# Kernel optimization log

Measured on AMD Instinct MI355X. Metric: run time of the kernel, lower is better.

Reference implementation:

```python
import jax, jax.numpy as jnp
import numpy as np

D_MODEL = 256
N_HEAD = 8
D_FF = 1024
B = 8
N_PER = 4096
NQ = B * N_PER
L = 16
NEG_INF = -1e9
EPS = 1e-5


def layer_norm(x, g, b):
    mu = jnp.mean(x, axis=-1, keepdims=True)
    var = jnp.mean(jnp.square(x - mu), axis=-1, keepdims=True)
    return (x - mu) * jax.lax.rsqrt(var + EPS) * g + b


def setup_inputs() -> dict:
    key = jax.random.key(0)
    ks = jax.random.split(key, 20)
    s = 1.0 / np.sqrt(D_MODEL)
    sf = 1.0 / np.sqrt(D_FF)
    inp = {
        "src": jax.random.normal(ks[0], (NQ, D_MODEL), jnp.float32),
        "pos": jax.random.normal(ks[1], (NQ, D_MODEL), jnp.float32),
        # per-batch-relative neighbor indices in [-1, N_PER); -1 == invalid/padded
        "index_pair": jax.random.randint(ks[2], (NQ, L), 0, N_PER + 1, jnp.int32) - 1,
        "query_batch_cnt": jnp.full((B,), N_PER, jnp.int32),
        "key_batch_cnt": jnp.full((B,), N_PER, jnp.int32),
        "index_pair_batch": (jnp.arange(NQ, dtype=jnp.int32) // N_PER).astype(jnp.int32),
        "Wq": jax.random.normal(ks[3], (D_MODEL, D_MODEL), jnp.float32) * s,
        "bq": jnp.zeros((D_MODEL,), jnp.float32),
        "Wk": jax.random.normal(ks[4], (D_MODEL, D_MODEL), jnp.float32) * s,
        "bk": jnp.zeros((D_MODEL,), jnp.float32),
        "Wv": jax.random.normal(ks[5], (D_MODEL, D_MODEL), jnp.float32) * s,
        "bv": jnp.zeros((D_MODEL,), jnp.float32),
        "Wo": jax.random.normal(ks[6], (D_MODEL, D_MODEL), jnp.float32) * s,
        "bo": jnp.zeros((D_MODEL,), jnp.float32),
        "W1": jax.random.normal(ks[7], (D_MODEL, D_FF), jnp.float32) * s,
        "b1": jnp.zeros((D_FF,), jnp.float32),
        "W2": jax.random.normal(ks[8], (D_FF, D_MODEL), jnp.float32) * sf,
        "b2": jnp.zeros((D_MODEL,), jnp.float32),
        "g1": jnp.ones((D_MODEL,), jnp.float32),
        "be1": jnp.zeros((D_MODEL,), jnp.float32),
        "g2": jnp.ones((D_MODEL,), jnp.float32),
        "be2": jnp.zeros((D_MODEL,), jnp.float32),
    }
    return inp


def local_attn(q, k, v, index_pair, key_batch_cnt, index_pair_batch,
               Wq, bq, Wk, bk, Wv, bv, Wo, bo):
    H, hd = N_HEAD, D_MODEL // N_HEAD
    scale = 1.0 / np.sqrt(hd)
    qh = (q @ Wq + bq).reshape(NQ, H, hd) * scale        # [Nq,H,hd]
    kh = (k @ Wk + bk).reshape(NQ, H, hd)                # [Nk,H,hd] (Nk==Nq)
    vh = (v @ Wv + bv).reshape(NQ, H, hd)
    # start offset of each batch's keys in the stacked key tensor
    offs = jnp.cumsum(key_batch_cnt) - key_batch_cnt      # [B]
    valid = index_pair >= 0                               # [Nq,L]
    gidx = jnp.where(valid, index_pair + offs[index_pair_batch][:, None], 0)
    k_g = kh[gidx]                                        # [Nq,L,H,hd]
    v_g = vh[gidx]                                        # [Nq,L,H,hd]
    logits = jnp.einsum('nhd,nlhd->nhl', qh, k_g)         # [Nq,H,L]
    logits = jnp.where(valid[:, None, :], logits, NEG_INF)
    attn = jax.nn.softmax(logits, axis=-1)
    out = jnp.einsum('nhl,nlhd->nhd', attn, v_g).reshape(NQ, D_MODEL)
    return out @ Wo + bo


def reference(src, pos, index_pair, query_batch_cnt, key_batch_cnt, index_pair_batch,
              Wq, bq, Wk, bk, Wv, bv, Wo, bo, W1, b1, W2, b2, g1, be1, g2, be2):
    # forward_post (normalize_before=False), dropout==0 (eval)
    qk = src + pos
    src2 = local_attn(qk, qk, src, index_pair, key_batch_cnt, index_pair_batch,
                      Wq, bq, Wk, bk, Wv, bv, Wo, bo)
    x = layer_norm(src + src2, g1, be1)
    ff = jax.nn.relu(x @ W1 + b1) @ W2 + b2
    return layer_norm(x + ff, g2, be2)
```

## Files before the change

kernel.cpp:

```cpp
#include <hip/hip_runtime.h>
#include <hip/hip_bf16.h>
#include <cstdint>
#include <cstddef>

#define NQ_ 32768
#define DM_ 256
#define DFF_ 1024
#define LNB_ 16
#define NB_ 8

typedef __attribute__((ext_vector_type(4))) float f32x4;
typedef __attribute__((ext_vector_type(8))) short s16x8;

__device__ __forceinline__ float bf2f(ushort u) {
    union { unsigned int i; float f; } c; c.i = ((unsigned int)u) << 16; return c.f;
}
__device__ __forceinline__ ushort f2bf(float f) {
    union { float f; unsigned int i; } c; c.f = f;
    unsigned int x = c.i;
    return (ushort)((x + 0x7fffu + ((x >> 16) & 1u)) >> 16);
}


__global__ __launch_bounds__(256) void prep_all(const float* __restrict__ src, const float* __restrict__ pos,
                                                ushort* __restrict__ qkb, ushort* __restrict__ srcb,
                                                const float* __restrict__ Wq, const float* __restrict__ Wk,
                                                const float* __restrict__ Wv, const float* __restrict__ Wo,
                                                const float* __restrict__ W1, const float* __restrict__ W2,
                                                const int* __restrict__ kbc,
                                                const float* __restrict__ bq, const float* __restrict__ bk,
                                                ushort* __restrict__ WqT, ushort* __restrict__ WkT,
                                                ushort* __restrict__ WvT, ushort* __restrict__ WoT,
                                                ushort* __restrict__ W1T, ushort* __restrict__ W2T,
                                                int* __restrict__ offs, float* __restrict__ bias2) {
    const int blk = blockIdx.x;
    const int t = threadIdx.x;
    if (blk < 8192) {
        const int i = (blk * 256 + t) * 4;
        float4 s = *(const float4*)(src + i);
        float4 p = *(const float4*)(pos + i);
        ushort4 a, b;
        a.x = f2bf(s.x + p.x); a.y = f2bf(s.y + p.y); a.z = f2bf(s.z + p.z); a.w = f2bf(s.w + p.w);
        b.x = f2bf(s.x);       b.y = f2bf(s.y);       b.z = f2bf(s.z);       b.w = f2bf(s.w);
        *(ushort4*)(qkb + i) = a;
        *(ushort4*)(srcb + i) = b;
        return;
    }
    const int b = blk - 8192;
    if (b == 3072) {
        if (t == 0) { int a = 0; for (int i = 0; i < NB_; ++i) { offs[i] = a; a += kbc[i]; } }
        bias2[t] = bq[t];
        bias2[256 + t] = bk[t];
        return;
    }
    const float* W; ushort* Wt; int base, ks, ns;
    if (b < 1024) {
        const int sec = b >> 8;
        W  = sec == 0 ? Wq  : sec == 1 ? Wk  : sec == 2 ? Wv  : Wo;
        Wt = sec == 0 ? WqT : sec == 1 ? WkT : sec == 2 ? WvT : WoT;
        base = (b & 255) * 256; ks = 8; ns = 8;
    } else if (b < 2048) {
        W = W1; Wt = W1T; base = (b - 1024) * 256; ks = 8; ns = 10;
    } else {
        W = W2; Wt = W2T; base = (b - 2048) * 256; ks = 10; ns = 8;
    }
    const int i = base + t;
    const int n = i >> ks, k = i & ((1 << ks) - 1);
    Wt[i] = f2bf(W[(k << ns) + n]);
}


__device__ __forceinline__ void gld_lds16(const ushort* g, ushort* l) {
    __builtin_amdgcn_global_load_lds((const __attribute__((address_space(1))) void*)g,
                                     (__attribute__((address_space(3))) void*)l, 16, 0, 0);
}

template <bool RELU>
__global__ __launch_bounds__(256) void gemm_kernel(const ushort* __restrict__ A, const ushort* __restrict__ Bt,
                                                   const float* __restrict__ bias, ushort* __restrict__ C,
                                                   int M, int N, int K, float alpha) {
    __shared__ __align__(16) ushort As[2 * 128 * 32];
    __shared__ __align__(16) ushort Bs[2 * 128 * 32];
    const int tid = threadIdx.x;
    const int lane = tid & 63;
    const int wave = tid >> 6;
    const int wr = wave >> 1, wc = wave & 1;

    const int b = (int)(blockIdx.y * gridDim.x + blockIdx.x);
    const int idx = b >> 3;
    const int xt = (b & 7) * 32 + (idx & 31);
    const int yt = idx >> 5;
    const long m0 = (long)xt * 128;
    const long n0 = (long)yt * 128;

    f32x4 acc[4][4] = {};

    const int c0 = tid, c1 = tid + 256;
    const int ar0 = c0 >> 2, ac0 = c0 & 3;
    const int ar1 = c1 >> 2, ac1 = c1 & 3;
    const int as0 = (ac0 ^ ((ar0 >> 1) & 3)) * 8;
    const int as1 = (ac1 ^ ((ar1 >> 1) & 3)) * 8;
    const int la = lane & 15;
    const int sx = ((lane >> 4) ^ ((la >> 1) & 3)) * 8;

    const ushort* Ar0 = A + (m0 + ar0) * K + as0;
    const ushort* Ar1 = A + (m0 + ar1) * K + as1;
    const ushort* Br0 = Bt + (n0 + ar0) * K + as0;
    const ushort* Br1 = Bt + (n0 + ar1) * K + as1;

    const int nt = K >> 5;
    int boff = 0;
    gld_lds16(Ar0, As + c0 * 8);
    gld_lds16(Ar1, As + c1 * 8);
    gld_lds16(Br0, Bs + c0 * 8);
    gld_lds16(Br1, Bs + c1 * 8);

    for (int t = 0; t < nt; ++t) {
        if (t + 1 < nt) {
            const int kt = (t + 1) << 5;
            const int nb = boff ^ 4096;
            gld_lds16(Ar0 + kt, As + nb + c0 * 8);
            gld_lds16(Ar1 + kt, As + nb + c1 * 8);
            gld_lds16(Br0 + kt, Bs + nb + c0 * 8);
            gld_lds16(Br1 + kt, Bs + nb + c1 * 8);
            asm volatile("s_waitcnt vmcnt(4)" ::: "memory");
        } else {
            asm volatile("s_waitcnt vmcnt(0)" ::: "memory");
        }
        __builtin_amdgcn_s_barrier();
        s16x8 af[4], bfr[4];
#pragma unroll
        for (int m = 0; m < 4; ++m)
            af[m] = *(const s16x8*)(As + boff + (wr * 64 + m * 16 + la) * 32 + sx);
#pragma unroll
        for (int n = 0; n < 4; ++n)
            bfr[n] = *(const s16x8*)(Bs + boff + (wc * 64 + n * 16 + la) * 32 + sx);
        asm volatile("s_waitcnt lgkmcnt(0)" ::: "memory");
        __builtin_amdgcn_s_barrier();
#pragma unroll
        for (int m = 0; m < 4; ++m)
#pragma unroll
            for (int n = 0; n < 4; ++n)
                acc[m][n] = __builtin_amdgcn_mfma_f32_16x16x32_bf16(af[m], bfr[n], acc[m][n], 0, 0, 0);
        boff ^= 4096;
    }

#pragma unroll
    for (int n = 0; n < 4; ++n) {
        const long col = n0 + wc * 64 + n * 16 + la;
        const float bv = bias[col];
#pragma unroll
        for (int m = 0; m < 4; ++m) {
#pragma unroll
            for (int j = 0; j < 4; ++j) {
                const long row = m0 + wr * 64 + m * 16 + (lane >> 4) * 4 + j;
                float r = (acc[m][n][j] + bv) * alpha;
                if (RELU) r = fmaxf(r, 0.f);
                C[row * N + col] = f2bf(r);
            }
        }
    }
}


__global__ __launch_bounds__(256) void qkv_kernel(const ushort* __restrict__ qkb, const ushort* __restrict__ srcb,
                                                  const ushort* __restrict__ WqkT, const ushort* __restrict__ WvT,
                                                  const float* __restrict__ bias2, const float* __restrict__ bv,
                                                  ushort* __restrict__ QKb, ushort* __restrict__ Vb) {
    __shared__ __align__(16) ushort As[2 * 128 * 32];
    __shared__ __align__(16) ushort Bs[2 * 128 * 32];
    const int tid = threadIdx.x;
    const int lane = tid & 63;
    const int wave = tid >> 6;
    const int wr = wave >> 1, wc = wave & 1;
    const int K = DM_;

    const bool isqk = blockIdx.y < 4;
    const ushort* A  = isqk ? qkb : srcb;
    const ushort* Bt = isqk ? WqkT : WvT;
    const float* bias = isqk ? bias2 : bv;
    ushort* C = isqk ? QKb : Vb;
    const int N = isqk ? 512 : 256;
    const int bx = (int)blockIdx.x;
    const int xt = (bx & 7) * 32 + (bx >> 3);
    const long m0 = (long)xt * 128;
    const long n0 = (long)(isqk ? blockIdx.y : (blockIdx.y - 4)) * 128;

    f32x4 acc[4][4] = {};

    const int c0 = tid, c1 = tid + 256;
    const int ar0 = c0 >> 2, ac0 = c0 & 3;
    const int ar1 = c1 >> 2, ac1 = c1 & 3;
    const int as0 = (ac0 ^ ((ar0 >> 1) & 3)) * 8;
    const int as1 = (ac1 ^ ((ar1 >> 1) & 3)) * 8;
    const int la = lane & 15;
    const int sx = ((lane >> 4) ^ ((la >> 1) & 3)) * 8;

    const ushort* Ar0 = A + (m0 + ar0) * K + as0;
    const ushort* Ar1 = A + (m0 + ar1) * K + as1;
    const ushort* Br0 = Bt + (n0 + ar0) * K + as0;
    const ushort* Br1 = Bt + (n0 + ar1) * K + as1;

    const int nt = K >> 5;
    int boff = 0;
    gld_lds16(Ar0, As + c0 * 8);
    gld_lds16(Ar1, As + c1 * 8);
    gld_lds16(Br0, Bs + c0 * 8);
    gld_lds16(Br1, Bs + c1 * 8);

    for (int t = 0; t < nt; ++t) {
        if (t + 1 < nt) {
            const int kt = (t + 1) << 5;
            const int nb = boff ^ 4096;
            gld_lds16(Ar0 + kt, As + nb + c0 * 8);
            gld_lds16(Ar1 + kt, As + nb + c1 * 8);
            gld_lds16(Br0 + kt, Bs + nb + c0 * 8);
            gld_lds16(Br1 + kt, Bs + nb + c1 * 8);
            asm volatile("s_waitcnt vmcnt(4)" ::: "memory");
        } else {
            asm volatile("s_waitcnt vmcnt(0)" ::: "memory");
        }
        __builtin_amdgcn_s_barrier();
        s16x8 af[4], bfr[4];
#pragma unroll
        for (int m = 0; m < 4; ++m)
            af[m] = *(const s16x8*)(As + boff + (wr * 64 + m * 16 + la) * 32 + sx);
#pragma unroll
        for (int n = 0; n < 4; ++n)
            bfr[n] = *(const s16x8*)(Bs + boff + (wc * 64 + n * 16 + la) * 32 + sx);
        asm volatile("s_waitcnt lgkmcnt(0)" ::: "memory");
        __builtin_amdgcn_s_barrier();
#pragma unroll
        for (int m = 0; m < 4; ++m)
#pragma unroll
            for (int n = 0; n < 4; ++n)
                acc[m][n] = __builtin_amdgcn_mfma_f32_16x16x32_bf16(af[m], bfr[n], acc[m][n], 0, 0, 0);
        boff ^= 4096;
    }

#pragma unroll
    for (int n = 0; n < 4; ++n) {
        const long col = n0 + wc * 64 + n * 16 + la;
        const float bvv = bias[col];
#pragma unroll
        for (int m = 0; m < 4; ++m) {
#pragma unroll
            for (int j = 0; j < 4; ++j) {
                const long row = m0 + wr * 64 + m * 16 + (lane >> 4) * 4 + j;
                C[row * N + col] = f2bf(acc[m][n][j] + bvv);
            }
        }
    }
}


template <bool F32OUT>
__global__ __launch_bounds__(256) void gemm_ln_kernel(const ushort* __restrict__ A, const ushort* __restrict__ Bt,
                                                      const float* __restrict__ bias,
                                                      const ushort* __restrict__ resid,
                                                      const float* __restrict__ g, const float* __restrict__ be,
                                                      void* __restrict__ outv, int K) {
    __shared__ __align__(16) ushort As[2 * 2 * 64 * 32];
    __shared__ __align__(16) ushort Bs[2 * 2 * 256 * 32];
    const int tid = threadIdx.x;
    const int lane = tid & 63;
    const int wave = tid >> 6;
    const long m0 = (long)blockIdx.x * 64;

    const int rel8 = ((tid & 3) ^ ((tid >> 3) & 3)) * 8;
    const int arow = tid >> 2;
    const ushort* Asrc = A + (m0 + arow) * K + rel8;
    const ushort* Bsrc[4];
#pragma unroll
    for (int j = 0; j < 4; ++j)
        Bsrc[j] = Bt + (long)(arow + 64 * j) * K + rel8;

    const int la = lane & 15;
    const int sx = ((lane >> 4) ^ ((la >> 1) & 3)) * 8;

    f32x4 acc[4][4] = {};
    const int nt = K >> 6;
    int buf = 0;
#pragma unroll
    for (int p = 0; p < 2; ++p)
        gld_lds16(Asrc + p * 32, As + (p * 256 + tid) * 8);
#pragma unroll
    for (int i = 0; i < 8; ++i)
        gld_lds16(Bsrc[i & 3] + (i >> 2) * 32, Bs + ((i >> 2) * 1024 + (i & 3) * 256 + tid) * 8);

    for (int t = 0; t < nt; ++t) {
        const int bA = buf * 4096, bB = buf * 16384;
        if (t + 1 < nt) {
            const int kt = (t + 1) << 6;
            const int nA = (buf ^ 1) * 4096, nB = (buf ^ 1) * 16384;
#pragma unroll
            for (int p = 0; p < 2; ++p)
                gld_lds16(Asrc + kt + p * 32, As + nA + (p * 256 + tid) * 8);
#pragma unroll
            for (int i = 0; i < 8; ++i)
                gld_lds16(Bsrc[i & 3] + kt + (i >> 2) * 32, Bs + nB + ((i >> 2) * 1024 + (i & 3) * 256 + tid) * 8);
            asm volatile("s_waitcnt vmcnt(10)" ::: "memory");
        } else {
            asm volatile("s_waitcnt vmcnt(0)" ::: "memory");
        }
        __builtin_amdgcn_s_barrier();
        s16x8 af[2][4], bfr[2][4];
#pragma unroll
        for (int kk = 0; kk < 2; ++kk) {
#pragma unroll
            for (int m = 0; m < 4; ++m)
                af[kk][m] = *(const s16x8*)(As + bA + kk * 2048 + (m * 16 + la) * 32 + sx);
#pragma unroll
            for (int n = 0; n < 4; ++n)
                bfr[kk][n] = *(const s16x8*)(Bs + bB + kk * 8192 + (wave * 64 + n * 16 + la) * 32 + sx);
        }
        asm volatile("s_waitcnt lgkmcnt(0)" ::: "memory");
        __builtin_amdgcn_s_barrier();
#pragma unroll
        for (int kk = 0; kk < 2; ++kk)
#pragma unroll
            for (int m = 0; m < 4; ++m)
#pragma unroll
                for (int n = 0; n < 4; ++n)
                    acc[m][n] = __builtin_amdgcn_mfma_f32_16x16x32_bf16(af[kk][m], bfr[kk][n], acc[m][n], 0, 0, 0);
        buf ^= 1;
    }

    float* red_s = (float*)As;
    float* red_q = (float*)As + 256;
    const int rg4 = (lane >> 4) * 4;
    float bv[4];
#pragma unroll
    for (int n = 0; n < 4; ++n) bv[n] = bias[wave * 64 + n * 16 + la];

#pragma unroll
    for (int m = 0; m < 4; ++m) {
#pragma unroll
        for (int j = 0; j < 4; ++j) {
            const int lr = m * 16 + rg4 + j;
            float s = 0.f, q = 0.f;
#pragma unroll
            for (int n = 0; n < 4; ++n) {
                const int col = wave * 64 + n * 16 + la;
                float v = acc[m][n][j] + bv[n] + bf2f(resid[(m0 + lr) * DM_ + col]);
                acc[m][n][j] = v;
                s += v; q += v * v;
            }
#pragma unroll
            for (int mk = 1; mk < 16; mk <<= 1) { s += __shfl_xor(s, mk); q += __shfl_xor(q, mk); }
            if (la == 0) { red_s[wave * 64 + lr] = s; red_q[wave * 64 + lr] = q; }
        }
    }
    __syncthreads();

    float gv[4], bev[4];
#pragma unroll
    for (int n = 0; n < 4; ++n) {
        const int col = wave * 64 + n * 16 + la;
        gv[n] = g[col]; bev[n] = be[col];
    }
#pragma unroll
    for (int m = 0; m < 4; ++m) {
#pragma unroll
        for (int j = 0; j < 4; ++j) {
            const int lr = m * 16 + rg4 + j;
            const float s = red_s[lr] + red_s[64 + lr] + red_s[128 + lr] + red_s[192 + lr];
            const float q = red_q[lr] + red_q[64 + lr] + red_q[128 + lr] + red_q[192 + lr];
            const float mu = s * (1.f / 256.f);
            const float rsig = rsqrtf(q * (1.f / 256.f) - mu * mu + 1e-5f);
#pragma unroll
            for (int n = 0; n < 4; ++n) {
                const int col = wave * 64 + n * 16 + la;
                const float r = (acc[m][n][j] - mu) * rsig * gv[n] + bev[n];
                if (F32OUT) ((float*)outv)[(m0 + lr) * DM_ + col] = r;
                else        ((ushort*)outv)[(m0 + lr) * DM_ + col] = f2bf(r);
            }
        }
    }
}


__global__ __launch_bounds__(256, 4) void attn_kernel(const ushort* __restrict__ QKb,
                                                      const ushort* __restrict__ Vb, const int* __restrict__ ipair,
                                                      const int* __restrict__ ipb, const int* __restrict__ offs,
                                                      ushort* __restrict__ Ob) {
    const int blk = (blockIdx.x & 7) * (NQ_ / 8 / 8) + (blockIdx.x >> 3);
    const int lane = threadIdx.x & 63;
    const int n = blk * 8 + (threadIdx.x >> 6) * 2 + (lane >> 5);
    const size_t hoff = (size_t)(lane & 31) * 8;

    float q[8];
    {
        s16x8 v = *(const s16x8*)(QKb + (size_t)n * 512 + hoff);
#pragma unroll
        for (int e = 0; e < 8; ++e) q[e] = bf2f((ushort)v[e]);
    }
    const int off = offs[ipb[n]];
    int gi[LNB_];
    float lg[LNB_];
#pragma unroll
    for (int j = 0; j < LNB_; ++j) {
        const int ip = ipair[n * LNB_ + j];
        const int g = ip >= 0 ? ip + off : 0;
        gi[j] = g;
        s16x8 v = *(const s16x8*)(QKb + (size_t)g * 512 + 256 + hoff);
        float p = 0.f;
#pragma unroll
        for (int e = 0; e < 8; ++e)
            p = fmaf(q[e], bf2f((ushort)v[e]), p);
        p += __shfl_xor(p, 1);
        p += __shfl_xor(p, 2);
        lg[j] = ip >= 0 ? p * 0.17677669529663688f : -1e9f;
    }
    float mx = lg[0];
#pragma unroll
    for (int j = 1; j < LNB_; ++j) mx = fmaxf(mx, lg[j]);
    float sum = 0.f, pw[LNB_];
#pragma unroll
    for (int j = 0; j < LNB_; ++j) { pw[j] = __expf(lg[j] - mx); sum += pw[j]; }
    const float inv = 1.f / sum;

    float acc[8] = {};
#pragma unroll
    for (int j = 0; j < LNB_; ++j) {
        s16x8 v = *(const s16x8*)(Vb + (size_t)gi[j] * DM_ + hoff);
        const float w = pw[j] * inv;
#pragma unroll
        for (int e = 0; e < 8; ++e)
            acc[e] = fmaf(w, bf2f((ushort)v[e]), acc[e]);
    }
    s16x8 o;
#pragma unroll
    for (int e = 0; e < 8; ++e) o[e] = (short)f2bf(acc[e]);
    *(s16x8*)(Ob + (size_t)n * DM_ + hoff) = o;
}


extern "C" void kernel_launch(void* const* d_in, const int* in_sizes, int n_in,
                              void* d_out, int out_size, void* d_ws, size_t ws_size,
                              hipStream_t stream) {
    const float* src = (const float*)d_in[0];
    const float* pos = (const float*)d_in[1];
    const int* ipair = (const int*)d_in[2];
    const int* kbc   = (const int*)d_in[4];
    const int* ipb   = (const int*)d_in[5];
    const float* Wq = (const float*)d_in[6];  const float* bq = (const float*)d_in[7];
    const float* Wk = (const float*)d_in[8];  const float* bk = (const float*)d_in[9];
    const float* Wv = (const float*)d_in[10]; const float* bv = (const float*)d_in[11];
    const float* Wo = (const float*)d_in[12]; const float* bo = (const float*)d_in[13];
    const float* W1 = (const float*)d_in[14]; const float* b1 = (const float*)d_in[15];
    const float* W2 = (const float*)d_in[16]; const float* b2 = (const float*)d_in[17];
    const float* g1 = (const float*)d_in[18]; const float* be1 = (const float*)d_in[19];
    const float* g2 = (const float*)d_in[20]; const float* be2 = (const float*)d_in[21];

    char* ws = (char*)d_ws;
    const size_t SB = (size_t)NQ_ * DM_ * 2;
    ushort* qkb  = (ushort*)(ws);
    ushort* srcb = (ushort*)(ws + SB);
    ushort* QKb  = (ushort*)(ws + 2 * SB);
    ushort* Vb   = (ushort*)(ws + 4 * SB);
    ushort* hb   = (ushort*)(ws);
    ushort* attno = qkb;
    ushort* xb    = Vb;
    char* wb = ws + 6 * SB;
    ushort* WqT = (ushort*)(wb);
    ushort* WkT = (ushort*)(wb + 131072);
    ushort* WvT = (ushort*)(wb + 262144);
    ushort* WoT = (ushort*)(wb + 393216);
    ushort* W1T = (ushort*)(wb + 524288);
    ushort* W2T = (ushort*)(wb + 1048576);
    int* offs   = (int*)(wb + 1572864);
    float* bias2 = (float*)(wb + 1572864 + 64);

    prep_all<<<8192 + 3073, 256, 0, stream>>>(src, pos, qkb, srcb,
                                              Wq, Wk, Wv, Wo, W1, W2, kbc, bq, bk,
                                              WqT, WkT, WvT, WoT, W1T, W2T, offs, bias2);

    dim3 gqkv(256, 6);
    dim3 gff1(NQ_ / 128, DFF_ / 128);
    qkv_kernel<<<gqkv, 256, 0, stream>>>(qkb, srcb, WqT, WvT, bias2, bv, QKb, Vb);
    attn_kernel<<<NQ_ / 8, 256, 0, stream>>>(QKb, Vb, ipair, ipb, offs, attno);
    gemm_ln_kernel<false><<<NQ_ / 64, 256, 0, stream>>>(attno, WoT, bo, srcb, g1, be1, (void*)xb, DM_);
    gemm_kernel<true><<<gff1, 256, 0, stream>>>(xb, W1T, b1, hb, NQ_, DFF_, DM_, 1.f);
    gemm_ln_kernel<true><<<NQ_ / 64, 256, 0, stream>>>(hb, W2T, b2, xb, g2, be2, d_out, DFF_);
}
```

Baseline: 172.2 us.

## Deepen GEMM K-step to 64 and prefetch V rows alongside K in attention

```diff
diff --git a/kernel.cpp b/kernel.cpp
--- a/kernel.cpp
+++ b/kernel.cpp
@@ -75,12 +75,13 @@
                                      (__attribute__((address_space(3))) void*)l, 16, 0, 0);
 }
 
+
 template <bool RELU>
 __global__ __launch_bounds__(256) void gemm_kernel(const ushort* __restrict__ A, const ushort* __restrict__ Bt,
                                                    const float* __restrict__ bias, ushort* __restrict__ C,
                                                    int M, int N, int K, float alpha) {
-    __shared__ __align__(16) ushort As[2 * 128 * 32];
-    __shared__ __align__(16) ushort Bs[2 * 128 * 32];
+    __shared__ __align__(16) ushort As[2 * 2 * 128 * 32];
+    __shared__ __align__(16) ushort Bs[2 * 2 * 128 * 32];
     const int tid = threadIdx.x;
     const int lane = tid & 63;
     const int wave = tid >> 6;
@@ -95,54 +96,61 @@
 
     f32x4 acc[4][4] = {};
 
-    const int c0 = tid, c1 = tid + 256;
-    const int ar0 = c0 >> 2, ac0 = c0 & 3;
-    const int ar1 = c1 >> 2, ac1 = c1 & 3;
-    const int as0 = (ac0 ^ ((ar0 >> 1) & 3)) * 8;
-    const int as1 = (ac1 ^ ((ar1 >> 1) & 3)) * 8;
+    const int rel8 = ((tid & 3) ^ ((tid >> 3) & 3)) * 8;
+    const ushort* Ar0 = A + (m0 + (tid >> 2)) * K + rel8;
+    const ushort* Ar1 = Ar0 + 64 * K;
+    const ushort* Br0 = Bt + (n0 + (tid >> 2)) * K + rel8;
+    const ushort* Br1 = Br0 + 64 * K;
     const int la = lane & 15;
     const int sx = ((lane >> 4) ^ ((la >> 1) & 3)) * 8;
 
-    const ushort* Ar0 = A + (m0 + ar0) * K + as0;
-    const ushort* Ar1 = A + (m0 + ar1) * K + as1;
-    const ushort* Br0 = Bt + (n0 + ar0) * K + as0;
-    const ushort* Br1 = Bt + (n0 + ar1) * K + as1;
-
-    const int nt = K >> 5;
-    int boff = 0;
-    gld_lds16(Ar0, As + c0 * 8);
-    gld_lds16(Ar1, As + c1 * 8);
-    gld_lds16(Br0, Bs + c0 * 8);
-    gld_lds16(Br1, Bs + c1 * 8);
+    const int nt = K >> 6;
+    int buf = 0;
+#pragma unroll
+    for (int p = 0; p < 2; ++p) {
+        gld_lds16(Ar0 + p * 32, As + p * 4096 + tid * 8);
+        gld_lds16(Ar1 + p * 32, As + p * 4096 + (tid + 256) * 8);
+        gld_lds16(Br0 + p * 32, Bs + p * 4096 + tid * 8);
+        gld_lds16(Br1 + p * 32, Bs + p * 4096 + (tid + 256) * 8);
+    }
 
     for (int t = 0; t < nt; ++t) {
+        const int bO = buf * 8192;
         if (t + 1 < nt) {
-            const int kt = (t + 1) << 5;
-            const int nb = boff ^ 4096;
-            gld_lds16(Ar0 + kt, As + nb + c0 * 8);
-            gld_lds16(Ar1 + kt, As + nb + c1 * 8);
-            gld_lds16(Br0 + kt, Bs + nb + c0 * 8);
-            gld_lds16(Br1 + kt, Bs + nb + c1 * 8);
-            asm volatile("s_waitcnt vmcnt(4)" ::: "memory");
+            const int kt = (t + 1) << 6;
+            const int nO = (buf ^ 1) * 8192;
+#pragma unroll
+            for (int p = 0; p < 2; ++p) {
+                gld_lds16(Ar0 + kt + p * 32, As + nO + p * 4096 + tid * 8);
+                gld_lds16(Ar1 + kt + p * 32, As + nO + p * 4096 + (tid + 256) * 8);
+                gld_lds16(Br0 + kt + p * 32, Bs + nO + p * 4096 + tid * 8);
+                gld_lds16(Br1 + kt + p * 32, Bs + nO + p * 4096 + (tid + 256) * 8);
+            }
+            asm volatile("s_waitcnt vmcnt(8)" ::: "memory");
         } else {
             asm volatile("s_waitcnt vmcnt(0)" ::: "memory");
         }
         __builtin_amdgcn_s_barrier();
-        s16x8 af[4], bfr[4];
-#pragma unroll
-        for (int m = 0; m < 4; ++m)
-            af[m] = *(const s16x8*)(As + boff + (wr * 64 + m * 16 + la) * 32 + sx);
-#pragma unroll
-        for (int n = 0; n < 4; ++n)
-            bfr[n] = *(const s16x8*)(Bs + boff + (wc * 64 + n * 16 + la) * 32 + sx);
+        s16x8 af[2][4], bfr[2][4];
+#pragma unroll
+        for (int kk = 0; kk < 2; ++kk) {
+#pragma unroll
+            for (int m = 0; m < 4; ++m)
+                af[kk][m] = *(const s16x8*)(As + bO + kk * 4096 + (wr * 64 + m * 16 + la) * 32 + sx);
+#pragma unroll
+            for (int n = 0; n < 4; ++n)
+                bfr[kk][n] = *(const s16x8*)(Bs + bO + kk * 4096 + (wc * 64 + n * 16 + la) * 32 + sx);
+        }
         asm volatile("s_waitcnt lgkmcnt(0)" ::: "memory");
         __builtin_amdgcn_s_barrier();
 #pragma unroll
-        for (int m = 0; m < 4; ++m)
-#pragma unroll
-            for (int n = 0; n < 4; ++n)
-                acc[m][n] = __builtin_amdgcn_mfma_f32_16x16x32_bf16(af[m], bfr[n], acc[m][n], 0, 0, 0);
-        boff ^= 4096;
+        for (int kk = 0; kk < 2; ++kk)
+#pragma unroll
+            for (int m = 0; m < 4; ++m)
+#pragma unroll
+                for (int n = 0; n < 4; ++n)
+                    acc[m][n] = __builtin_amdgcn_mfma_f32_16x16x32_bf16(af[kk][m], bfr[kk][n], acc[m][n], 0, 0, 0);
+        buf ^= 1;
     }
 
 #pragma unroll
@@ -167,8 +175,8 @@
                                                   const ushort* __restrict__ WqkT, const ushort* __restrict__ WvT,
                                                   const float* __restrict__ bias2, const float* __restrict__ bv,
                                                   ushort* __restrict__ QKb, ushort* __restrict__ Vb) {
-    __shared__ __align__(16) ushort As[2 * 128 * 32];
-    __shared__ __align__(16) ushort Bs[2 * 128 * 32];
+    __shared__ __align__(16) ushort As[2 * 2 * 128 * 32];
+    __shared__ __align__(16) ushort Bs[2 * 2 * 128 * 32];
     const int tid = threadIdx.x;
     const int lane = tid & 63;
     const int wave = tid >> 6;
@@ -188,54 +196,61 @@
 
     f32x4 acc[4][4] = {};
 
-    const int c0 = tid, c1 = tid + 256;
-    const int ar0 = c0 >> 2, ac0 = c0 & 3;
-    const int ar1 = c1 >> 2, ac1 = c1 & 3;
-    const int as0 = (ac0 ^ ((ar0 >> 1) & 3)) * 8;
-    const int as1 = (ac1 ^ ((ar1 >> 1) & 3)) * 8;
+    const int rel8 = ((tid & 3) ^ ((tid >> 3) & 3)) * 8;
+    const ushort* Ar0 = A + (m0 + (tid >> 2)) * K + rel8;
+    const ushort* Ar1 = Ar0 + 64 * K;
+    const ushort* Br0 = Bt + (n0 + (tid >> 2)) * K + rel8;
+    const ushort* Br1 = Br0 + 64 * K;
     const int la = lane & 15;
     const int sx = ((lane >> 4) ^ ((la >> 1) & 3)) * 8;
 
-    const ushort* Ar0 = A + (m0 + ar0) * K + as0;
-    const ushort* Ar1 = A + (m0 + ar1) * K + as1;
-    const ushort* Br0 = Bt + (n0 + ar0) * K + as0;
-    const ushort* Br1 = Bt + (n0 + ar1) * K + as1;
-
-    const int nt = K >> 5;
-    int boff = 0;
-    gld_lds16(Ar0, As + c0 * 8);
-    gld_lds16(Ar1, As + c1 * 8);
-    gld_lds16(Br0, Bs + c0 * 8);
-    gld_lds16(Br1, Bs + c1 * 8);
+    const int nt = K >> 6;
+    int buf = 0;
+#pragma unroll
+    for (int p = 0; p < 2; ++p) {
+        gld_lds16(Ar0 + p * 32, As + p * 4096 + tid * 8);
+        gld_lds16(Ar1 + p * 32, As + p * 4096 + (tid + 256) * 8);
+        gld_lds16(Br0 + p * 32, Bs + p * 4096 + tid * 8);
+        gld_lds16(Br1 + p * 32, Bs + p * 4096 + (tid + 256) * 8);
+    }
 
     for (int t = 0; t < nt; ++t) {
+        const int bO = buf * 8192;
         if (t + 1 < nt) {
-            const int kt = (t + 1) << 5;
-            const int nb = boff ^ 4096;
-            gld_lds16(Ar0 + kt, As + nb + c0 * 8);
-            gld_lds16(Ar1 + kt, As + nb + c1 * 8);
-            gld_lds16(Br0 + kt, Bs + nb + c0 * 8);
-            gld_lds16(Br1 + kt, Bs + nb + c1 * 8);
-            asm volatile("s_waitcnt vmcnt(4)" ::: "memory");
+            const int kt = (t + 1) << 6;
+            const int nO = (buf ^ 1) * 8192;
+#pragma unroll
+            for (int p = 0; p < 2; ++p) {
+                gld_lds16(Ar0 + kt + p * 32, As + nO + p * 4096 + tid * 8);
+                gld_lds16(Ar1 + kt + p * 32, As + nO + p * 4096 + (tid + 256) * 8);
+                gld_lds16(Br0 + kt + p * 32, Bs + nO + p * 4096 + tid * 8);
+                gld_lds16(Br1 + kt + p * 32, Bs + nO + p * 4096 + (tid + 256) * 8);
+            }
+            asm volatile("s_waitcnt vmcnt(8)" ::: "memory");
         } else {
             asm volatile("s_waitcnt vmcnt(0)" ::: "memory");
         }
         __builtin_amdgcn_s_barrier();
-        s16x8 af[4], bfr[4];
-#pragma unroll
-        for (int m = 0; m < 4; ++m)
-            af[m] = *(const s16x8*)(As + boff + (wr * 64 + m * 16 + la) * 32 + sx);
-#pragma unroll
-        for (int n = 0; n < 4; ++n)
-            bfr[n] = *(const s16x8*)(Bs + boff + (wc * 64 + n * 16 + la) * 32 + sx);
+        s16x8 af[2][4], bfr[2][4];
+#pragma unroll
+        for (int kk = 0; kk < 2; ++kk) {
+#pragma unroll
+            for (int m = 0; m < 4; ++m)
+                af[kk][m] = *(const s16x8*)(As + bO + kk * 4096 + (wr * 64 + m * 16 + la) * 32 + sx);
+#pragma unroll
+            for (int n = 0; n < 4; ++n)
+                bfr[kk][n] = *(const s16x8*)(Bs + bO + kk * 4096 + (wc * 64 + n * 16 + la) * 32 + sx);
+        }
         asm volatile("s_waitcnt lgkmcnt(0)" ::: "memory");
         __builtin_amdgcn_s_barrier();
 #pragma unroll
-        for (int m = 0; m < 4; ++m)
-#pragma unroll
-            for (int n = 0; n < 4; ++n)
-                acc[m][n] = __builtin_amdgcn_mfma_f32_16x16x32_bf16(af[m], bfr[n], acc[m][n], 0, 0, 0);
-        boff ^= 4096;
+        for (int kk = 0; kk < 2; ++kk)
+#pragma unroll
+            for (int m = 0; m < 4; ++m)
+#pragma unroll
+                for (int n = 0; n < 4; ++n)
+                    acc[m][n] = __builtin_amdgcn_mfma_f32_16x16x32_bf16(af[kk][m], bfr[kk][n], acc[m][n], 0, 0, 0);
+        buf ^= 1;
     }
 
 #pragma unroll
@@ -380,7 +395,7 @@
 }
 
 
-__global__ __launch_bounds__(256, 4) void attn_kernel(const ushort* __restrict__ QKb,
+__global__ __launch_bounds__(256, 3) void attn_kernel(const ushort* __restrict__ QKb,
                                                       const ushort* __restrict__ Vb, const int* __restrict__ ipair,
                                                       const int* __restrict__ ipb, const int* __restrict__ offs,
                                                       ushort* __restrict__ Ob) {
@@ -396,14 +411,14 @@
         for (int e = 0; e < 8; ++e) q[e] = bf2f((ushort)v[e]);
     }
     const int off = offs[ipb[n]];
-    int gi[LNB_];
     float lg[LNB_];
+    s16x8 va[LNB_];
 #pragma unroll
     for (int j = 0; j < LNB_; ++j) {
         const int ip = ipair[n * LNB_ + j];
         const int g = ip >= 0 ? ip + off : 0;
-        gi[j] = g;
         s16x8 v = *(const s16x8*)(QKb + (size_t)g * 512 + 256 + hoff);
+        va[j] = *(const s16x8*)(Vb + (size_t)g * DM_ + hoff);
         float p = 0.f;
 #pragma unroll
         for (int e = 0; e < 8; ++e)
@@ -423,11 +438,10 @@
     float acc[8] = {};
 #pragma unroll
     for (int j = 0; j < LNB_; ++j) {
-        s16x8 v = *(const s16x8*)(Vb + (size_t)gi[j] * DM_ + hoff);
         const float w = pw[j] * inv;
 #pragma unroll
         for (int e = 0; e < 8; ++e)
-            acc[e] = fmaf(w, bf2f((ushort)v[e]), acc[e]);
+            acc[e] = fmaf(w, bf2f((ushort)va[j][e]), acc[e]);
     }
     s16x8 o;
 #pragma unroll
```

Result: faster. 165.1 us (-4.1%).
